# Kernel optimization log

Measured on AMD Instinct MI355X. Metric: run time of the kernel, lower is better.

The kernel has to match this reference:

```python
import jax, jax.numpy as jnp
import numpy as np

# DeepSeek MLA prefill pipeline (absorbed form), matching the GEMM/bmm/sparse-attention
# Dims: m=512 tokens, hidden=7168, d_kv_c=512, d_q_c=1536, d_r=64, d_q=d_kv=128,
# h=16 local heads, attention dim d = d_kv_c + d_r = 576, s_kv=4096, topk=512.

M, HID = 512, 7168
D_KV_C, D_Q_C, D_R, D_Q, D_KV = 512, 1536, 64, 128, 128
H = 16
S_KV, TOPK = 4096, 512
D_ATT = D_KV_C + D_R  # 576


def setup_inputs() -> dict:
    key = jax.random.key(0)
    ks = jax.random.split(key, 8)
    s = lambda n: 1.0 / np.sqrt(n).astype(np.float32)
    return {
        "x": jax.random.normal(ks[0], (M, HID), jnp.float32),
        "W_cqkv": jax.random.normal(ks[1], (HID, D_KV_C + D_Q_C + D_R), jnp.float32) * s(HID),
        "W_uq": jax.random.normal(ks[2], (D_Q_C, H * (D_Q + D_R)), jnp.float32) * s(D_Q_C),
        "W_qk": jax.random.normal(ks[3], (H, D_Q, D_KV_C), jnp.float32) * s(D_Q),
        "kv_cache": jax.random.normal(ks[4], (S_KV, D_ATT), jnp.float32),
        "W_o1": jax.random.normal(ks[5], (H, D_KV_C, D_KV), jnp.float32) * s(D_KV_C),
        "W_oproj": jax.random.normal(ks[6], (H * D_KV, HID), jnp.float32) * s(H * D_KV),
        "indices": jax.random.randint(ks[7], (M, TOPK), 0, S_KV, jnp.int32),
    }


def reference(x, W_cqkv, W_uq, W_qk, kv_cache, W_o1, W_oproj, indices):
    # 1) QKV compression GEMM: [m, hid] @ [hid, d_kv_c + d_q_c + d_r]
    c = x @ W_cqkv
    kv_c_new = c[:, :D_KV_C]                      # compressed KV (would extend cache)
    q_c = c[:, D_KV_C:D_KV_C + D_Q_C]             # [m, d_q_c]
    # (kv_c_new / k_r_new feed the cache in a real pipeline; attention below reads

    # 2) Q uncompression GEMM: [m, d_q_c] @ [d_q_c, h*(d_q+d_r)]
    q = (q_c @ W_uq).reshape(M, H, D_Q + D_R)
    q_nope, q_pe = q[..., :D_Q], q[..., D_Q:]     # [m,h,128], [m,h,64]

    # 3) Q absorb bmm: per-head [m, d_q] @ [d_q, d_kv_c]
    q_abs = jnp.einsum('mhq,hqc->mhc', q_nope, W_qk)
    q_full = jnp.concatenate([q_abs, q_pe], axis=-1)  # [m, h, 576]

    # 4) Top-k sparse MLA attention (flash_mla_sparse_fwd math):
    #    indices shared across heads (h_kv = 1); gather kv rows per query token.
    kv_g = kv_cache[indices]                      # [m, topk, 576]
    sm_scale = 1.0 / jnp.sqrt(jnp.float32(D_ATT))
    scores = jnp.einsum('mhd,mtd->mht', q_full, kv_g) * sm_scale
    attn = jax.nn.softmax(scores, axis=-1)        # [m, h, topk]
    o = jnp.einsum('mht,mtc->mhc', attn, kv_g[..., :D_KV_C])  # value = first d_kv_c dims

    # 5) O bmm: per-head [m, d_kv_c] @ [d_kv_c, d_kv]
    o2 = jnp.einsum('mhc,hcv->mhv', o, W_o1)      # [m, h, 128]

    # 6) O projection GEMM: [m, h*d_kv] @ [h*d_kv, hid]
    out = o2.reshape(M, H * D_KV) @ W_oproj       # [m, hid]
    return out
```

## Files before the change

### kernel.cpp

```cpp
#include <hip/hip_runtime.h>
#include <hip/hip_bf16.h>

#define M_DIM 512
#define HID 7168
#define D_KV_C 512
#define D_Q_C 1536
#define D_R 64
#define D_Q 128
#define D_KV 128
#define H_DIM 16
#define S_KV 4096
#define TOPK 512
#define D_ATT 576
#define SPLIT 2
#define SROWS 256
#define SM_SCALE (1.0f / 24.0f)

typedef _Float16 half_t;
typedef __attribute__((ext_vector_type(8))) _Float16 f16x8_t;
typedef __attribute__((ext_vector_type(4))) float f32x4_t;
typedef __attribute__((ext_vector_type(2))) unsigned int u32x2_t;

#define MFMA_F16(a, b, c) __builtin_amdgcn_mfma_f32_16x16x32_f16((a), (b), (c), 0, 0, 0)

__device__ __forceinline__ unsigned lds_addr32(const void* p) {
    return (unsigned)(unsigned long long)(const __attribute__((address_space(3))) char*)p;
}

typedef const __attribute__((address_space(1))) unsigned int* gptr_t;
typedef __attribute__((address_space(3))) unsigned int* lptr_t;
__device__ __forceinline__ void gload_lds16(const void* g, void* l) {
    __builtin_amdgcn_global_load_lds((gptr_t)g, (lptr_t)l, 16, 0, 0);
}

__global__ __launch_bounds__(256) void cvt_f16(const float* __restrict__ src,
                                               half_t* __restrict__ dst, int n8)
{
    int i = blockIdx.x * 256 + threadIdx.x;
    if (i >= n8) return;
    const float4* s = (const float4*)src + (size_t)i * 2;
    float4 a = s[0], b = s[1];
    f16x8_t o;
    o[0] = (half_t)a.x; o[1] = (half_t)a.y; o[2] = (half_t)a.z; o[3] = (half_t)a.w;
    o[4] = (half_t)b.x; o[5] = (half_t)b.y; o[6] = (half_t)b.z; o[7] = (half_t)b.w;
    *(f16x8_t*)(dst + (size_t)i * 8) = o;
}

template<int NS>
__global__ __launch_bounds__(256) void cvt_sum(const float* __restrict__ src, long long slice,
                                               half_t* __restrict__ dst, int n8)
{
    int i = blockIdx.x * 256 + threadIdx.x;
    if (i >= n8) return;
    float a[8] = {};
    #pragma unroll
    for (int s = 0; s < NS; s++) {
        const float4* p = (const float4*)(src + (size_t)s * slice) + (size_t)i * 2;
        float4 u = p[0], v = p[1];
        a[0] += u.x; a[1] += u.y; a[2] += u.z; a[3] += u.w;
        a[4] += v.x; a[5] += v.y; a[6] += v.z; a[7] += v.w;
    }
    f16x8_t o;
    #pragma unroll
    for (int j = 0; j < 8; j++) o[j] = (half_t)a[j];
    *(f16x8_t*)(dst + (size_t)i * 8) = o;
}

__global__ __launch_bounds__(256) void cvt_sum_q(const float* __restrict__ src, long long slice,
                                                 half_t* __restrict__ q16, half_t* __restrict__ qf)
{
    int i = blockIdx.x * 256 + threadIdx.x;
    if (i >= M_DIM * 3072 / 8) return;
    float a[8] = {};
    #pragma unroll
    for (int s = 0; s < 2; s++) {
        const float4* p = (const float4*)(src + (size_t)s * slice) + (size_t)i * 2;
        float4 u = p[0], v = p[1];
        a[0] += u.x; a[1] += u.y; a[2] += u.z; a[3] += u.w;
        a[4] += v.x; a[5] += v.y; a[6] += v.z; a[7] += v.w;
    }
    f16x8_t o;
    #pragma unroll
    for (int j = 0; j < 8; j++) o[j] = (half_t)a[j];
    *(f16x8_t*)(q16 + (size_t)i * 8) = o;
    int col = (i * 8) % 3072;
    int c = col % 192;
    if (c >= 128) {
        int row = (i * 8) / 3072, h = col / 192;
        int mh = row * 16 + h;
        f16x8_t os;
        #pragma unroll
        for (int j = 0; j < 8; j++) os[j] = (half_t)(a[j] * SM_SCALE);
        *(f16x8_t*)(qf + (size_t)mh * D_ATT + D_KV_C + (c - 128)) = os;
    }
}

__global__ __launch_bounds__(256) void cvt_t(
    const float* __restrict__ src, int ld_src, long long sS,
    half_t* __restrict__ dst, int ld_dst, long long sD)
{
    src += (size_t)blockIdx.z * sS;
    dst += (size_t)blockIdx.z * sD;
    int k0 = blockIdx.y * 64, n0 = blockIdx.x * 64;
    __shared__ half_t t[64][80];
    int tid = threadIdx.x;
    int kr = tid >> 4, nc = (tid & 15) * 4;
    #pragma unroll
    for (int i = 0; i < 4; i++) {
        float4 v = *(const float4*)&src[(size_t)(k0 + kr + i * 16) * ld_src + n0 + nc];
        t[nc + 0][kr + i * 16] = (half_t)v.x;
        t[nc + 1][kr + i * 16] = (half_t)v.y;
        t[nc + 2][kr + i * 16] = (half_t)v.z;
        t[nc + 3][kr + i * 16] = (half_t)v.w;
    }
    __syncthreads();
    int nr = tid >> 2, kc = (tid & 3) * 16;
    f16x8_t w0 = *(const f16x8_t*)&t[nr][kc];
    f16x8_t w1 = *(const f16x8_t*)&t[nr][kc + 8];
    *(f16x8_t*)&dst[(size_t)(n0 + nr) * ld_dst + k0 + kc] = w0;
    *(f16x8_t*)&dst[(size_t)(n0 + nr) * ld_dst + k0 + kc + 8] = w1;
}

template<bool F16OUT>
__global__ __launch_bounds__(256) void gemm_f16t(
    const half_t* __restrict__ A, int lda, long long sA,
    const half_t* __restrict__ Bt, int ldb, long long sB,
    void* __restrict__ Cv, int ldc, long long sC, int K, float alpha)
{
    A  += (size_t)blockIdx.z * sA;
    Bt += (size_t)blockIdx.z * sB;
    const int bm = blockIdx.y * 64, bn = blockIdx.x * 64;

    __shared__ __align__(16) char lds[2][16384];

    const int tid = threadIdx.x, w = tid >> 6, lane = tid & 63;
    const int l15 = lane & 15, q = lane >> 4;
    const int wr = w >> 1, wc = w & 1;

    const half_t* gA[2];
    const half_t* gB[2];
    #pragma unroll
    for (int p = 0; p < 2; p++) {
        int c = p * 64 + lane;
        int rl = c >> 3;
        int sg = (c & 7) ^ (rl & 7);
        gA[p] = A  + (size_t)(bm + w * 16 + rl) * lda + sg * 8;
        gB[p] = Bt + (size_t)(bn + w * 16 + rl) * ldb + sg * 8;
    }

    f32x4_t acc[2][2];
    #pragma unroll
    for (int i = 0; i < 2; i++)
        #pragma unroll
        for (int j = 0; j < 2; j++) acc[i][j] = (f32x4_t){0.f, 0.f, 0.f, 0.f};

    const int nsteps = K >> 6;

    {
        char* ab = lds[0];
        char* bb = ab + 8192;
        #pragma unroll
        for (int p = 0; p < 2; p++) {
            gload_lds16(gA[p], ab + w * 2048 + p * 1024);
            gload_lds16(gB[p], bb + w * 2048 + p * 1024);
        }
    }
    __syncthreads();

    int cur = 0;
    for (int s = 0; s < nsteps; s++) {
        if (s + 1 < nsteps) {
            int k0 = (s + 1) << 6;
            char* ab = lds[cur ^ 1];
            char* bb = ab + 8192;
            #pragma unroll
            for (int p = 0; p < 2; p++) {
                gload_lds16(gA[p] + k0, ab + w * 2048 + p * 1024);
                gload_lds16(gB[p] + k0, bb + w * 2048 + p * 1024);
            }
        }
        {
            const char* ab = lds[cur];
            const char* bb = ab + 8192;
            #pragma unroll
            for (int kk = 0; kk < 2; kk++) {
                f16x8_t av[2], bv[2];
                #pragma unroll
                for (int i = 0; i < 2; i++) {
                    int ra = wr * 32 + i * 16 + l15;
                    av[i] = *(const f16x8_t*)(ab + ra * 128 + (((kk * 4 + q) ^ (ra & 7)) * 16));
                    int rb = wc * 32 + i * 16 + l15;
                    bv[i] = *(const f16x8_t*)(bb + rb * 128 + (((kk * 4 + q) ^ (rb & 7)) * 16));
                }
                #pragma unroll
                for (int i = 0; i < 2; i++)
                    #pragma unroll
                    for (int j = 0; j < 2; j++)
                        acc[i][j] = MFMA_F16(av[i], bv[j], acc[i][j]);
            }
        }
        __syncthreads();
        cur ^= 1;
    }

    half_t* Ch = (half_t*)Cv + (F16OUT ? (size_t)blockIdx.z * sC : 0);
    float*  Cf = (float*)Cv  + (F16OUT ? 0 : (size_t)blockIdx.z * sC);
    #pragma unroll
    for (int i = 0; i < 2; i++)
        #pragma unroll
        for (int j = 0; j < 2; j++)
            #pragma unroll
            for (int r = 0; r < 4; r++) {
                size_t row = bm + wr * 32 + i * 16 + q * 4 + r;
                size_t col = bn + wc * 32 + j * 16 + l15;
                float v = acc[i][j][r] * alpha;
                if (F16OUT) Ch[row * ldc + col] = (half_t)v;
                else        Cf[row * ldc + col] = v;
            }
}

__global__ __launch_bounds__(512, 4) void attn_split(
    const half_t* __restrict__ qf,
    const half_t* __restrict__ kvb,
    const int* __restrict__ indices,
    half_t* __restrict__ op,
    float2* __restrict__ ml)
{
    const int m = blockIdx.x, sp = blockIdx.y;
    const int tid = threadIdx.x;
    const int w = tid >> 6, lane = tid & 63;
    const int l15 = lane & 15, q = lane >> 4;

    __shared__ __align__(16) char vbuf[2][32768];
    __shared__ __align__(16) unsigned short p_s[16 * SROWS];
    __shared__ float red_m[16][8];
    __shared__ float red_s[16][8];

    const int* idxp = indices + (size_t)m * TOPK + sp * SROWS;

    {
        #pragma unroll
        for (int j = 0; j < 4; j++) {
            int R = 4 * w + j;
            int grow = idxp[R];
            unsigned swz = (((unsigned)(R & 7)) << 4) ^ (((unsigned)((R >> 3) & 3)) << 5);
            const char* src = (const char*)(kvb + (size_t)grow * D_ATT) + (((unsigned)(16 * lane)) ^ swz);
            gload_lds16(src, vbuf[0] + R * 1024);
        }
    }

    const int rows0 = idxp[(w * 2 + 0) * 16 + l15];
    const int rows1 = idxp[(w * 2 + 1) * 16 + l15];

    f32x4_t acc0 = (f32x4_t){0.f, 0.f, 0.f, 0.f};
    f32x4_t acc1 = (f32x4_t){0.f, 0.f, 0.f, 0.f};

    const half_t* qp  = qf  + ((size_t)m * 16 + l15) * D_ATT + q * 8;
    const half_t* kp0 = kvb + (size_t)rows0 * D_ATT + q * 8;
    const half_t* kp1 = kvb + (size_t)rows1 * D_ATT + q * 8;

    #pragma unroll
    for (int kk = 0; kk < 18; kk++) {
        f16x8_t ah = *(const f16x8_t*)(qp  + kk * 32);
        f16x8_t b0 = *(const f16x8_t*)(kp0 + kk * 32);
        f16x8_t b1 = *(const f16x8_t*)(kp1 + kk * 32);
        acc0 = MFMA_F16(ah, b0, acc0);
        acc1 = MFMA_F16(ah, b1, acc1);
    }

    float gm[4], e0[4], e1[4];
    #pragma unroll
    for (int r = 0; r < 4; r++) {
        float mx = fmaxf(acc0[r], acc1[r]);
        #pragma unroll
        for (int off = 8; off; off >>= 1) mx = fmaxf(mx, __shfl_xor(mx, off, 16));
        if (l15 == 0) red_m[q * 4 + r][w] = mx;
    }
    __syncthreads();
    #pragma unroll
    for (int r = 0; r < 4; r++) {
        int h = q * 4 + r;
        float mx = red_m[h][0];
        #pragma unroll
        for (int ww = 1; ww < 8; ww++) mx = fmaxf(mx, red_m[h][ww]);
        gm[r] = mx;
        e0[r] = __expf(acc0[r] - mx);
        e1[r] = __expf(acc1[r] - mx);
        float s = e0[r] + e1[r];
        #pragma unroll
        for (int off = 8; off; off >>= 1) s += __shfl_xor(s, off, 16);
        if (l15 == 0) red_s[h][w] = s;
    }
    __syncthreads();
    if (w == 0 && l15 == 0) {
        #pragma unroll
        for (int r = 0; r < 4; r++) {
            int h = q * 4 + r;
            float s = 0.f;
            #pragma unroll
            for (int ww = 0; ww < 8; ww++) s += red_s[h][ww];
            ml[(size_t)sp * (M_DIM * H_DIM) + m * 16 + h] = make_float2(gm[r], s);
        }
    }
    #pragma unroll
    for (int r = 0; r < 4; r++) {
        int h = q * 4 + r;
        int t0 = (w * 2 + 0) * 16 + l15;
        int t1 = t0 + 16;
        union { half_t hh; unsigned short u; } c0, c1;
        c0.hh = (half_t)e0[r]; c1.hh = (half_t)e1[r];
        p_s[h * SROWS + ((((unsigned)(t0 * 2)) ^ (((unsigned)(h & 7)) << 4)) >> 1)] = c0.u;
        p_s[h * SROWS + ((((unsigned)(t1 * 2)) ^ (((unsigned)(h & 7)) << 4)) >> 1)] = c1.u;
    }
    __syncthreads();

    f32x4_t oacc[4];
    #pragma unroll
    for (int i = 0; i < 4; i++) oacc[i] = (f32x4_t){0.f, 0.f, 0.f, 0.f};

    const int row1 = q * 8 + (l15 >> 2);
    const int row2 = row1 + 4;
    const unsigned sw1 = (((unsigned)(row1 & 7)) << 4) ^ (((unsigned)((row1 >> 3) & 3)) << 5);
    const unsigned sw2 = (((unsigned)(row2 & 7)) << 4) ^ (((unsigned)((row2 >> 3) & 3)) << 5);
    const unsigned cbyte = (unsigned)((l15 & 3) * 8);

    #pragma unroll 1
    for (int ct = 0; ct < 8; ct++) {
        if (ct < 7) {
            #pragma unroll
            for (int j = 0; j < 4; j++) {
                int R = 4 * w + j;
                int grow = idxp[(ct + 1) * 32 + R];
                unsigned swz = (((unsigned)(R & 7)) << 4) ^ (((unsigned)((R >> 3) & 3)) << 5);
                const char* src = (const char*)(kvb + (size_t)grow * D_ATT) + (((unsigned)(16 * lane)) ^ swz);
                gload_lds16(src, vbuf[(ct + 1) & 1] + R * 1024);
            }
        }

        const unsigned vb = lds_addr32(vbuf[ct & 1]);

        f16x8_t pa;
        {
            unsigned pbyte = ((unsigned)(ct * 64 + q * 16)) ^ (((unsigned)(l15 & 7)) << 4);
            pa = *(const f16x8_t*)((const char*)p_s + l15 * (SROWS * 2) + pbyte);
        }

        u32x2_t blo[4], bhi[4];
        #pragma unroll
        for (int i = 0; i < 4; i++) {
            unsigned c2 = ((unsigned)((w * 4 + i) * 32)) + cbyte;
            unsigned a1 = vb + (unsigned)row1 * 1024u + (c2 ^ sw1);
            unsigned a2 = vb + (unsigned)row2 * 1024u + (c2 ^ sw2);
            asm volatile("ds_read_b64_tr_b16 %0, %1 offset:0" : "=v"(blo[i]) : "v"(a1) : "memory");
            asm volatile("ds_read_b64_tr_b16 %0, %1 offset:0" : "=v"(bhi[i]) : "v"(a2) : "memory");
        }
        asm volatile("s_waitcnt lgkmcnt(0)" ::: "memory");
        __builtin_amdgcn_sched_barrier(0);

        __builtin_amdgcn_s_setprio(1);
        #pragma unroll
        for (int i = 0; i < 4; i++) {
            union { f16x8_t s; struct { u32x2_t lo, hi; } u; } f;
            f.u.lo = blo[i]; f.u.hi = bhi[i];
            oacc[i] = MFMA_F16(pa, f.s, oacc[i]);
        }
        __builtin_amdgcn_s_setprio(0);

        __syncthreads();
    }

    half_t* ob = op + ((size_t)sp * M_DIM + m) * (H_DIM * D_KV_C);
    #pragma unroll
    for (int i = 0; i < 4; i++) {
        int c = (w * 4 + i) * 16 + l15;
        #pragma unroll
        for (int r = 0; r < 4; r++)
            ob[(size_t)(q * 4 + r) * D_KV_C + c] = (half_t)oacc[i][r];
    }
}

__global__ __launch_bounds__(256) void attn_merge(
    const half_t* __restrict__ op,
    const float2* __restrict__ ml,
    half_t* __restrict__ o)
{
    int idx = blockIdx.x * 256 + threadIdx.x;
    if (idx >= M_DIM * H_DIM * D_KV_C / 8) return;
    int mh = idx >> 6;
    int c8 = (idx & 63) * 8;
    float2 a = ml[mh];
    float2 b = ml[M_DIM * H_DIM + mh];
    float Mx = fmaxf(a.x, b.x);
    float w0 = __expf(a.x - Mx), w1 = __expf(b.x - Mx);
    float inv = 1.0f / (w0 * a.y + w1 * b.y);
    w0 *= inv; w1 *= inv;
    f16x8_t v0 = *(const f16x8_t*)(op + (size_t)mh * D_KV_C + c8);
    f16x8_t v1 = *(const f16x8_t*)(op + ((size_t)(M_DIM * H_DIM) + mh) * D_KV_C + c8);
    f16x8_t o8;
    #pragma unroll
    for (int j = 0; j < 8; j++)
        o8[j] = (half_t)(w0 * (float)v0[j] + w1 * (float)v1[j]);
    *(f16x8_t*)(o + (size_t)mh * D_KV_C + c8) = o8;
}

extern "C" void kernel_launch(void* const* d_in, const int* in_sizes, int n_in,
                              void* d_out, int out_size, void* d_ws, size_t ws_size,
                              hipStream_t stream)
{
    const float* x        = (const float*)d_in[0];
    const float* W_cqkv   = (const float*)d_in[1];
    const float* W_uq     = (const float*)d_in[2];
    const float* W_qk     = (const float*)d_in[3];
    const float* kv_cache = (const float*)d_in[4];
    const float* W_o1     = (const float*)d_in[5];
    const float* W_oproj  = (const float*)d_in[6];
    const int*   indices  = (const int*)d_in[7];
    float* out = (float*)d_out;

    half_t* wsh = (half_t*)d_ws;
    half_t* Wcqkv_t = wsh;
    half_t* qc16    = wsh;
    half_t* o_part  = wsh;
    half_t* q32h    = wsh + 786432;
    half_t* q16     = wsh + 7077888;
    half_t* x16     = wsh + 11010048;
    half_t* o2_16   = wsh + 11010048;
    half_t* Wuq_t   = wsh + 14680064;
    half_t* o16     = wsh + 14680064;
    half_t* Wqk_t   = wsh + 19398656;
    half_t* ml_h    = wsh + 19398656;
    half_t* Wo1_t   = wsh + 20447232;
    half_t* Wop_t   = wsh + 21495808;
    half_t* kv16    = wsh + 36175872;
    half_t* qc32h   = wsh + 38535168;
    half_t* qf16    = wsh + 38535168;
    float*  qc32 = (float*)qc32h;
    float*  q32  = (float*)q32h;
    float2* ml   = (float2*)ml_h;

    cvt_f16<<<(M_DIM * HID / 8 + 255) / 256, 256, 0, stream>>>(x, x16, M_DIM * HID / 8);
    cvt_f16<<<(S_KV * D_ATT / 8 + 255) / 256, 256, 0, stream>>>(kv_cache, kv16, S_KV * D_ATT / 8);
    cvt_t<<<dim3(D_Q_C / 64, HID / 64, 1), 256, 0, stream>>>(
        W_cqkv + D_KV_C, D_KV_C + D_Q_C + D_R, 0, Wcqkv_t, HID, 0);
    cvt_t<<<dim3(3072 / 64, D_Q_C / 64, 1), 256, 0, stream>>>(
        W_uq, 3072, 0, Wuq_t, D_Q_C, 0);
    cvt_t<<<dim3(D_KV_C / 64, D_Q / 64, H_DIM), 256, 0, stream>>>(
        W_qk, D_KV_C, D_Q * D_KV_C, Wqk_t, D_Q, D_Q * D_KV_C);
    cvt_t<<<dim3(D_KV / 64, D_KV_C / 64, H_DIM), 256, 0, stream>>>(
        W_o1, D_KV, D_KV_C * D_KV, Wo1_t, D_KV_C, D_KV_C * D_KV);
    cvt_t<<<dim3(HID / 64, 2048 / 64, 1), 256, 0, stream>>>(
        W_oproj, HID, 0, Wop_t, 2048, 0);

    gemm_f16t<false><<<dim3(D_Q_C / 64, M_DIM / 64, 4), 256, 0, stream>>>(
        x16, HID, 1792, Wcqkv_t, HID, 1792, qc32, D_Q_C, (long long)M_DIM * D_Q_C, 1792, 1.0f);
    cvt_sum<4><<<(M_DIM * D_Q_C / 8 + 255) / 256, 256, 0, stream>>>(
        qc32, (long long)M_DIM * D_Q_C, qc16, M_DIM * D_Q_C / 8);

    gemm_f16t<false><<<dim3(3072 / 64, M_DIM / 64, 2), 256, 0, stream>>>(
        qc16, D_Q_C, 768, Wuq_t, D_Q_C, 768, q32, 3072, (long long)M_DIM * 3072, 768, 1.0f);
    cvt_sum_q<<<(M_DIM * 3072 / 8 + 255) / 256, 256, 0, stream>>>(
        q32, (long long)M_DIM * 3072, q16, qf16);

    gemm_f16t<true><<<dim3(D_KV_C / 64, M_DIM / 64, H_DIM), 256, 0, stream>>>(
        q16, 3072, D_Q + D_R, Wqk_t, D_Q, (long long)D_Q * D_KV_C,
        qf16, H_DIM * D_ATT, D_ATT, D_Q, SM_SCALE);

    attn_split<<<dim3(M_DIM, SPLIT), 512, 0, stream>>>(qf16, kv16, indices, o_part, ml);
    attn_merge<<<(M_DIM * H_DIM * D_KV_C / 8 + 255) / 256, 256, 0, stream>>>(o_part, ml, o16);

    gemm_f16t<true><<<dim3(D_KV / 64, M_DIM / 64, H_DIM), 256, 0, stream>>>(
        o16, H_DIM * D_KV_C, D_KV_C, Wo1_t, D_KV_C, (long long)D_KV_C * D_KV,
        o2_16, H_DIM * D_KV, D_KV, D_KV_C, 1.0f);

    gemm_f16t<false><<<dim3(HID / 64, M_DIM / 64, 1), 256, 0, stream>>>(
        o2_16, H_DIM * D_KV, 0, Wop_t, 2048, 0, out, HID, 0, 2048, 1.0f);
}
```

Baseline: 215.9 us.

## Split attention into four KV chunks with single-buffered LDS and in-place merge

```diff
diff --git a/kernel.cpp b/kernel.cpp
--- a/kernel.cpp
+++ b/kernel.cpp
@@ -12,8 +12,8 @@
 #define S_KV 4096
 #define TOPK 512
 #define D_ATT 576
-#define SPLIT 2
-#define SROWS 256
+#define SPLIT 4
+#define SROWS 128
 #define SM_SCALE (1.0f / 24.0f)
 
 typedef _Float16 half_t;
@@ -219,7 +219,7 @@
             }
 }
 
-__global__ __launch_bounds__(512, 4) void attn_split(
+__global__ __launch_bounds__(512, 8) void attn_split(
     const half_t* __restrict__ qf,
     const half_t* __restrict__ kvb,
     const int* __restrict__ indices,
@@ -231,7 +231,7 @@
     const int w = tid >> 6, lane = tid & 63;
     const int l15 = lane & 15, q = lane >> 4;
 
-    __shared__ __align__(16) char vbuf[2][32768];
+    __shared__ __align__(16) char vbuf[32768];
     __shared__ __align__(16) unsigned short p_s[16 * SROWS];
     __shared__ float red_m[16][8];
     __shared__ float red_s[16][8];
@@ -245,33 +245,28 @@
             int grow = idxp[R];
             unsigned swz = (((unsigned)(R & 7)) << 4) ^ (((unsigned)((R >> 3) & 3)) << 5);
             const char* src = (const char*)(kvb + (size_t)grow * D_ATT) + (((unsigned)(16 * lane)) ^ swz);
-            gload_lds16(src, vbuf[0] + R * 1024);
-        }
-    }
-
-    const int rows0 = idxp[(w * 2 + 0) * 16 + l15];
-    const int rows1 = idxp[(w * 2 + 1) * 16 + l15];
+            gload_lds16(src, vbuf + R * 1024);
+        }
+    }
+
+    const int rows0 = idxp[w * 16 + l15];
 
     f32x4_t acc0 = (f32x4_t){0.f, 0.f, 0.f, 0.f};
-    f32x4_t acc1 = (f32x4_t){0.f, 0.f, 0.f, 0.f};
 
     const half_t* qp  = qf  + ((size_t)m * 16 + l15) * D_ATT + q * 8;
     const half_t* kp0 = kvb + (size_t)rows0 * D_ATT + q * 8;
-    const half_t* kp1 = kvb + (size_t)rows1 * D_ATT + q * 8;
 
     #pragma unroll
     for (int kk = 0; kk < 18; kk++) {
         f16x8_t ah = *(const f16x8_t*)(qp  + kk * 32);
         f16x8_t b0 = *(const f16x8_t*)(kp0 + kk * 32);
-        f16x8_t b1 = *(const f16x8_t*)(kp1 + kk * 32);
         acc0 = MFMA_F16(ah, b0, acc0);
-        acc1 = MFMA_F16(ah, b1, acc1);
-    }
-
-    float gm[4], e0[4], e1[4];
+    }
+
+    float gm[4], e0[4];
     #pragma unroll
     for (int r = 0; r < 4; r++) {
-        float mx = fmaxf(acc0[r], acc1[r]);
+        float mx = acc0[r];
         #pragma unroll
         for (int off = 8; off; off >>= 1) mx = fmaxf(mx, __shfl_xor(mx, off, 16));
         if (l15 == 0) red_m[q * 4 + r][w] = mx;
@@ -285,8 +280,7 @@
         for (int ww = 1; ww < 8; ww++) mx = fmaxf(mx, red_m[h][ww]);
         gm[r] = mx;
         e0[r] = __expf(acc0[r] - mx);
-        e1[r] = __expf(acc1[r] - mx);
-        float s = e0[r] + e1[r];
+        float s = e0[r];
         #pragma unroll
         for (int off = 8; off; off >>= 1) s += __shfl_xor(s, off, 16);
         if (l15 == 0) red_s[h][w] = s;
@@ -305,12 +299,10 @@
     #pragma unroll
     for (int r = 0; r < 4; r++) {
         int h = q * 4 + r;
-        int t0 = (w * 2 + 0) * 16 + l15;
-        int t1 = t0 + 16;
-        union { half_t hh; unsigned short u; } c0, c1;
-        c0.hh = (half_t)e0[r]; c1.hh = (half_t)e1[r];
+        int t0 = w * 16 + l15;
+        union { half_t hh; unsigned short u; } c0;
+        c0.hh = (half_t)e0[r];
         p_s[h * SROWS + ((((unsigned)(t0 * 2)) ^ (((unsigned)(h & 7)) << 4)) >> 1)] = c0.u;
-        p_s[h * SROWS + ((((unsigned)(t1 * 2)) ^ (((unsigned)(h & 7)) << 4)) >> 1)] = c1.u;
     }
     __syncthreads();
 
@@ -323,50 +315,50 @@
     const unsigned sw1 = (((unsigned)(row1 & 7)) << 4) ^ (((unsigned)((row1 >> 3) & 3)) << 5);
     const unsigned sw2 = (((unsigned)(row2 & 7)) << 4) ^ (((unsigned)((row2 >> 3) & 3)) << 5);
     const unsigned cbyte = (unsigned)((l15 & 3) * 8);
+    const unsigned vb = lds_addr32(vbuf);
 
     #pragma unroll 1
-    for (int ct = 0; ct < 8; ct++) {
-        if (ct < 7) {
+    for (int ct = 0; ct < SPLIT; ct++) {
+        f16x8_t pa;
+        {
+            unsigned pbyte = ((unsigned)(ct * 64 + q * 16)) ^ (((unsigned)(l15 & 7)) << 4);
+            pa = *(const f16x8_t*)((const char*)p_s + l15 * (SROWS * 2) + pbyte);
+        }
+
+        u32x2_t blo[4], bhi[4];
+        #pragma unroll
+        for (int i = 0; i < 4; i++) {
+            unsigned c2 = ((unsigned)((w * 4 + i) * 32)) + cbyte;
+            unsigned a1 = vb + (unsigned)row1 * 1024u + (c2 ^ sw1);
+            unsigned a2 = vb + (unsigned)row2 * 1024u + (c2 ^ sw2);
+            asm volatile("ds_read_b64_tr_b16 %0, %1 offset:0" : "=v"(blo[i]) : "v"(a1) : "memory");
+            asm volatile("ds_read_b64_tr_b16 %0, %1 offset:0" : "=v"(bhi[i]) : "v"(a2) : "memory");
+        }
+        asm volatile("s_waitcnt lgkmcnt(0)" ::: "memory");
+        __builtin_amdgcn_sched_barrier(0);
+
+        __builtin_amdgcn_s_setprio(1);
+        #pragma unroll
+        for (int i = 0; i < 4; i++) {
+            union { f16x8_t s; struct { u32x2_t lo, hi; } u; } f;
+            f.u.lo = blo[i]; f.u.hi = bhi[i];
+            oacc[i] = MFMA_F16(pa, f.s, oacc[i]);
+        }
+        __builtin_amdgcn_s_setprio(0);
+
+        __syncthreads();
+
+        if (ct < SPLIT - 1) {
             #pragma unroll
             for (int j = 0; j < 4; j++) {
                 int R = 4 * w + j;
                 int grow = idxp[(ct + 1) * 32 + R];
                 unsigned swz = (((unsigned)(R & 7)) << 4) ^ (((unsigned)((R >> 3) & 3)) << 5);
                 const char* src = (const char*)(kvb + (size_t)grow * D_ATT) + (((unsigned)(16 * lane)) ^ swz);
-                gload_lds16(src, vbuf[(ct + 1) & 1] + R * 1024);
+                gload_lds16(src, vbuf + R * 1024);
             }
-        }
-
-        const unsigned vb = lds_addr32(vbuf[ct & 1]);
-
-        f16x8_t pa;
-        {
-            unsigned pbyte = ((unsigned)(ct * 64 + q * 16)) ^ (((unsigned)(l15 & 7)) << 4);
-            pa = *(const f16x8_t*)((const char*)p_s + l15 * (SROWS * 2) + pbyte);
-        }
-
-        u32x2_t blo[4], bhi[4];
-        #pragma unroll
-        for (int i = 0; i < 4; i++) {
-            unsigned c2 = ((unsigned)((w * 4 + i) * 32)) + cbyte;
-            unsigned a1 = vb + (unsigned)row1 * 1024u + (c2 ^ sw1);
-            unsigned a2 = vb + (unsigned)row2 * 1024u + (c2 ^ sw2);
-            asm volatile("ds_read_b64_tr_b16 %0, %1 offset:0" : "=v"(blo[i]) : "v"(a1) : "memory");
-            asm volatile("ds_read_b64_tr_b16 %0, %1 offset:0" : "=v"(bhi[i]) : "v"(a2) : "memory");
-        }
-        asm volatile("s_waitcnt lgkmcnt(0)" ::: "memory");
-        __builtin_amdgcn_sched_barrier(0);
-
-        __builtin_amdgcn_s_setprio(1);
-        #pragma unroll
-        for (int i = 0; i < 4; i++) {
-            union { f16x8_t s; struct { u32x2_t lo, hi; } u; } f;
-            f.u.lo = blo[i]; f.u.hi = bhi[i];
-            oacc[i] = MFMA_F16(pa, f.s, oacc[i]);
-        }
-        __builtin_amdgcn_s_setprio(0);
-
-        __syncthreads();
+            __syncthreads();
+        }
     }
 
     half_t* ob = op + ((size_t)sp * M_DIM + m) * (H_DIM * D_KV_C);
@@ -380,27 +372,35 @@
 }
 
 __global__ __launch_bounds__(256) void attn_merge(
-    const half_t* __restrict__ op,
-    const float2* __restrict__ ml,
-    half_t* __restrict__ o)
+    half_t* __restrict__ op,
+    const float2* __restrict__ ml)
 {
     int idx = blockIdx.x * 256 + threadIdx.x;
     if (idx >= M_DIM * H_DIM * D_KV_C / 8) return;
     int mh = idx >> 6;
     int c8 = (idx & 63) * 8;
-    float2 a = ml[mh];
-    float2 b = ml[M_DIM * H_DIM + mh];
-    float Mx = fmaxf(a.x, b.x);
-    float w0 = __expf(a.x - Mx), w1 = __expf(b.x - Mx);
-    float inv = 1.0f / (w0 * a.y + w1 * b.y);
-    w0 *= inv; w1 *= inv;
-    f16x8_t v0 = *(const f16x8_t*)(op + (size_t)mh * D_KV_C + c8);
-    f16x8_t v1 = *(const f16x8_t*)(op + ((size_t)(M_DIM * H_DIM) + mh) * D_KV_C + c8);
+    float2 a[SPLIT];
+    #pragma unroll
+    for (int s = 0; s < SPLIT; s++) a[s] = ml[s * (M_DIM * H_DIM) + mh];
+    float Mx = a[0].x;
+    #pragma unroll
+    for (int s = 1; s < SPLIT; s++) Mx = fmaxf(Mx, a[s].x);
+    float ws[SPLIT], denom = 0.f;
+    #pragma unroll
+    for (int s = 0; s < SPLIT; s++) { ws[s] = __expf(a[s].x - Mx); denom += ws[s] * a[s].y; }
+    float inv = 1.0f / denom;
+    float acc[8] = {};
+    #pragma unroll
+    for (int s = 0; s < SPLIT; s++) {
+        f16x8_t v = *(const f16x8_t*)(op + ((size_t)s * (M_DIM * H_DIM) + mh) * D_KV_C + c8);
+        float wn = ws[s] * inv;
+        #pragma unroll
+        for (int j = 0; j < 8; j++) acc[j] += wn * (float)v[j];
+    }
     f16x8_t o8;
     #pragma unroll
-    for (int j = 0; j < 8; j++)
-        o8[j] = (half_t)(w0 * (float)v0[j] + w1 * (float)v1[j]);
-    *(f16x8_t*)(o + (size_t)mh * D_KV_C + c8) = o8;
+    for (int j = 0; j < 8; j++) o8[j] = (half_t)acc[j];
+    *(f16x8_t*)(op + (size_t)mh * D_KV_C + c8) = o8;
 }
 
 extern "C" void kernel_launch(void* const* d_in, const int* in_sizes, int n_in,
@@ -421,12 +421,12 @@
     half_t* Wcqkv_t = wsh;
     half_t* qc16    = wsh;
     half_t* o_part  = wsh;
+    half_t* o16     = wsh;
     half_t* q32h    = wsh + 786432;
     half_t* q16     = wsh + 7077888;
     half_t* x16     = wsh + 11010048;
-    half_t* o2_16   = wsh + 11010048;
     half_t* Wuq_t   = wsh + 14680064;
-    half_t* o16     = wsh + 14680064;
+    half_t* o2_16   = wsh + 16777216;
     half_t* Wqk_t   = wsh + 19398656;
     half_t* ml_h    = wsh + 19398656;
     half_t* Wo1_t   = wsh + 20447232;
@@ -466,7 +466,7 @@
         qf16, H_DIM * D_ATT, D_ATT, D_Q, SM_SCALE);
 
     attn_split<<<dim3(M_DIM, SPLIT), 512, 0, stream>>>(qf16, kv16, indices, o_part, ml);
-    attn_merge<<<(M_DIM * H_DIM * D_KV_C / 8 + 255) / 256, 256, 0, stream>>>(o_part, ml, o16);
+    attn_merge<<<(M_DIM * H_DIM * D_KV_C / 8 + 255) / 256, 256, 0, stream>>>(o_part, ml);
 
     gemm_f16t<true><<<dim3(D_KV / 64, M_DIM / 64, H_DIM), 256, 0, stream>>>(
         o16, H_DIM * D_KV_C, D_KV_C, Wo1_t, D_KV_C, (long long)D_KV_C * D_KV,
```

Measured after the change: 232.7 us. 1.08x slower.

## Add 128x128-tile GEMM kernel and use it for large GEMMs

Applied to the files above, without the earlier changes.

```diff
diff --git a/kernel.cpp b/kernel.cpp
--- a/kernel.cpp
+++ b/kernel.cpp
@@ -66,6 +66,7 @@
     *(f16x8_t*)(dst + (size_t)i * 8) = o;
 }
 
+template<int NS>
 __global__ __launch_bounds__(256) void cvt_sum_q(const float* __restrict__ src, long long slice,
                                                  half_t* __restrict__ q16, half_t* __restrict__ qf)
 {
@@ -73,7 +74,7 @@
     if (i >= M_DIM * 3072 / 8) return;
     float a[8] = {};
     #pragma unroll
-    for (int s = 0; s < 2; s++) {
+    for (int s = 0; s < NS; s++) {
         const float4* p = (const float4*)(src + (size_t)s * slice) + (size_t)i * 2;
         float4 u = p[0], v = p[1];
         a[0] += u.x; a[1] += u.y; a[2] += u.z; a[3] += u.w;
@@ -219,6 +220,107 @@
             }
 }
 
+template<bool F16OUT>
+__global__ __launch_bounds__(512, 4) void gemm_f16t_big(
+    const half_t* __restrict__ A, int lda, long long sA,
+    const half_t* __restrict__ Bt, int ldb, long long sB,
+    void* __restrict__ Cv, int ldc, long long sC, int K, float alpha)
+{
+    A  += (size_t)blockIdx.z * sA;
+    Bt += (size_t)blockIdx.z * sB;
+    const int bm = blockIdx.y * 128, bn = blockIdx.x * 128;
+
+    __shared__ __align__(16) char lds[2][32768];
+
+    const int tid = threadIdx.x, w = tid >> 6, lane = tid & 63;
+    const int l15 = lane & 15, q = lane >> 4;
+    const int wr = w >> 2, wc = w & 3;
+
+    const half_t* gA[2];
+    const half_t* gB[2];
+    #pragma unroll
+    for (int p = 0; p < 2; p++) {
+        int c = p * 64 + lane;
+        int rl = c >> 3;
+        int sg = (c & 7) ^ (rl & 7);
+        gA[p] = A  + (size_t)(bm + w * 16 + rl) * lda + sg * 8;
+        gB[p] = Bt + (size_t)(bn + w * 16 + rl) * ldb + sg * 8;
+    }
+
+    f32x4_t acc[4][2];
+    #pragma unroll
+    for (int i = 0; i < 4; i++)
+        #pragma unroll
+        for (int j = 0; j < 2; j++) acc[i][j] = (f32x4_t){0.f, 0.f, 0.f, 0.f};
+
+    const int nsteps = K >> 6;
+
+    {
+        char* ab = lds[0];
+        char* bb = ab + 16384;
+        #pragma unroll
+        for (int p = 0; p < 2; p++) {
+            gload_lds16(gA[p], ab + w * 2048 + p * 1024);
+            gload_lds16(gB[p], bb + w * 2048 + p * 1024);
+        }
+    }
+    __syncthreads();
+
+    int cur = 0;
+    for (int s = 0; s < nsteps; s++) {
+        if (s + 1 < nsteps) {
+            int k0 = (s + 1) << 6;
+            char* ab = lds[cur ^ 1];
+            char* bb = ab + 16384;
+            #pragma unroll
+            for (int p = 0; p < 2; p++) {
+                gload_lds16(gA[p] + k0, ab + w * 2048 + p * 1024);
+                gload_lds16(gB[p] + k0, bb + w * 2048 + p * 1024);
+            }
+        }
+        {
+            const char* ab = lds[cur];
+            const char* bb = ab + 16384;
+            #pragma unroll
+            for (int kk = 0; kk < 2; kk++) {
+                f16x8_t av[4], bv[2];
+                #pragma unroll
+                for (int i = 0; i < 4; i++) {
+                    int ra = wr * 64 + i * 16 + l15;
+                    av[i] = *(const f16x8_t*)(ab + ra * 128 + (((kk * 4 + q) ^ (ra & 7)) * 16));
+                }
+                #pragma unroll
+                for (int j = 0; j < 2; j++) {
+                    int rb = wc * 32 + j * 16 + l15;
+                    bv[j] = *(const f16x8_t*)(bb + rb * 128 + (((kk * 4 + q) ^ (rb & 7)) * 16));
+                }
+                #pragma unroll
+                for (int i = 0; i < 4; i++)
+                    #pragma unroll
+                    for (int j = 0; j < 2; j++)
+                        acc[i][j] = MFMA_F16(av[i], bv[j], acc[i][j]);
+            }
+        }
+        __syncthreads();
+        cur ^= 1;
+    }
+
+    half_t* Ch = (half_t*)Cv + (F16OUT ? (size_t)blockIdx.z * sC : 0);
+    float*  Cf = (float*)Cv  + (F16OUT ? 0 : (size_t)blockIdx.z * sC);
+    #pragma unroll
+    for (int i = 0; i < 4; i++)
+        #pragma unroll
+        for (int j = 0; j < 2; j++)
+            #pragma unroll
+            for (int r = 0; r < 4; r++) {
+                size_t row = bm + wr * 64 + i * 16 + q * 4 + r;
+                size_t col = bn + wc * 32 + j * 16 + l15;
+                float v = acc[i][j][r] * alpha;
+                if (F16OUT) Ch[row * ldc + col] = (half_t)v;
+                else        Cf[row * ldc + col] = v;
+            }
+}
+
 __global__ __launch_bounds__(512, 4) void attn_split(
     const half_t* __restrict__ qf,
     const half_t* __restrict__ kvb,
@@ -422,7 +524,7 @@
     half_t* qc16    = wsh;
     half_t* o_part  = wsh;
     half_t* q32h    = wsh + 786432;
-    half_t* q16     = wsh + 7077888;
+    half_t* q16     = wsh + 13369344;
     half_t* x16     = wsh + 11010048;
     half_t* o2_16   = wsh + 11010048;
     half_t* Wuq_t   = wsh + 14680064;
@@ -451,14 +553,14 @@
     cvt_t<<<dim3(HID / 64, 2048 / 64, 1), 256, 0, stream>>>(
         W_oproj, HID, 0, Wop_t, 2048, 0);
 
-    gemm_f16t<false><<<dim3(D_Q_C / 64, M_DIM / 64, 4), 256, 0, stream>>>(
+    gemm_f16t_big<false><<<dim3(D_Q_C / 128, M_DIM / 128, 4), 512, 0, stream>>>(
         x16, HID, 1792, Wcqkv_t, HID, 1792, qc32, D_Q_C, (long long)M_DIM * D_Q_C, 1792, 1.0f);
     cvt_sum<4><<<(M_DIM * D_Q_C / 8 + 255) / 256, 256, 0, stream>>>(
         qc32, (long long)M_DIM * D_Q_C, qc16, M_DIM * D_Q_C / 8);
 
-    gemm_f16t<false><<<dim3(3072 / 64, M_DIM / 64, 2), 256, 0, stream>>>(
-        qc16, D_Q_C, 768, Wuq_t, D_Q_C, 768, q32, 3072, (long long)M_DIM * 3072, 768, 1.0f);
-    cvt_sum_q<<<(M_DIM * 3072 / 8 + 255) / 256, 256, 0, stream>>>(
+    gemm_f16t_big<false><<<dim3(3072 / 128, M_DIM / 128, 4), 512, 0, stream>>>(
+        qc16, D_Q_C, 384, Wuq_t, D_Q_C, 384, q32, 3072, (long long)M_DIM * 3072, 384, 1.0f);
+    cvt_sum_q<4><<<(M_DIM * 3072 / 8 + 255) / 256, 256, 0, stream>>>(
         q32, (long long)M_DIM * 3072, q16, qf16);
 
     gemm_f16t<true><<<dim3(D_KV_C / 64, M_DIM / 64, H_DIM), 256, 0, stream>>>(
@@ -472,6 +574,6 @@
         o16, H_DIM * D_KV_C, D_KV_C, Wo1_t, D_KV_C, (long long)D_KV_C * D_KV,
         o2_16, H_DIM * D_KV, D_KV, D_KV_C, 1.0f);
 
-    gemm_f16t<false><<<dim3(HID / 64, M_DIM / 64, 1), 256, 0, stream>>>(
+    gemm_f16t_big<false><<<dim3(HID / 128, M_DIM / 128, 1), 512, 0, stream>>>(
         o2_16, H_DIM * D_KV, 0, Wop_t, 2048, 0, out, HID, 0, 2048, 1.0f);
 }
```

New measurement: 222.6 us. +3.1%, slower.
